# Performance work log

Measured on AMD Instinct MI355X. Metric: run time of the kernel, lower is better.

Reference implementation:

```python
import jax, jax.numpy as jnp
import numpy as np

HIDDEN = 2048
INTER = 7168
N_EXPERTS = 8
BATCH, SEQ, TOP_K = 1, 2048, 2


def setup_inputs() -> dict:
    key = jax.random.key(0)
    ks = jax.random.split(key, 6)
    x = jax.random.normal(ks[0], (BATCH, SEQ, HIDDEN), dtype=jnp.float32)
    expert_indices = jax.random.randint(ks[1], (BATCH, SEQ, TOP_K), 0, N_EXPERTS, dtype=jnp.int64)
    expert_weights = jax.random.uniform(ks[2], (BATCH, SEQ, TOP_K), dtype=jnp.float32)
    gate_proj = jax.random.normal(ks[3], (N_EXPERTS, INTER, HIDDEN), dtype=jnp.float32) * 0.02
    up_proj = jax.random.normal(ks[4], (N_EXPERTS, INTER, HIDDEN), dtype=jnp.float32) * 0.02
    down_proj = jax.random.normal(ks[5], (N_EXPERTS, HIDDEN, INTER), dtype=jnp.float32) * 0.02
    return {"x": x, "expert_indices": expert_indices, "expert_weights": expert_weights,
            "gate_proj": gate_proj, "up_proj": up_proj, "down_proj": down_proj}


def reference(x, expert_indices, expert_weights, gate_proj, up_proj, down_proj):
    B, S, H = x.shape
    E = gate_proj.shape[0]
    T = B * S
    xf = x.reshape(T, H)
    # Per-token combine weight for each expert: sum router weights over the
    # top-k slots that picked that expert.  comb: [T, E]
    onehot = jax.nn.one_hot(expert_indices.reshape(T, -1), E, dtype=x.dtype)  # [T, K, E]
    comb = jnp.einsum('tke,tk->te', onehot, expert_weights.reshape(T, -1))
    out = jnp.zeros((T, H), dtype=x.dtype)
    for e in range(E):  # small fixed loop over experts (structurally distinct weights)
        g = xf @ gate_proj[e].T            # [T, I]
        u = xf @ up_proj[e].T              # [T, I]
        h = g * jax.nn.sigmoid(g) * u      # SwiGLU (silu(gate) * up)
        out = out + (h @ down_proj[e].T) * comb[:, e:e + 1]
    return out.reshape(B, S, H)
```

## Files before the change

### kernel.cpp

```cpp
#include <hip/hip_runtime.h>
#include <hip/hip_bf16.h>
#include <math.h>

#define HDIM 2048
#define IDIM 7168
#define NEXP 8
#define TTOK 2048
#define TOPK 2
#define NASSIGN (TTOK * TOPK)
#define ROWCAP 5120

#define BK 32
#define LDK 40

typedef float  f32x4 __attribute__((ext_vector_type(4)));
typedef int    i32x4 __attribute__((ext_vector_type(4)));
typedef unsigned short u16;
typedef u16    u16x8 __attribute__((ext_vector_type(8)));

__device__ __forceinline__ u16 f2bf(float f) {
    return __builtin_bit_cast(u16, (__bf16)f);
}

__device__ __forceinline__ f32x4 mfma16(i32x4 a, i32x4 b, f32x4 c) {
    asm("v_mfma_f32_16x16x32_bf16 %0, %1, %2, %0" : "+v"(c) : "v"(a), "v"(b));
    return c;
}

__device__ __forceinline__ void cvt_store8(u16* dst, f32x4 a, f32x4 b) {
    u16x8 p;
    p[0]=f2bf(a[0]); p[1]=f2bf(a[1]); p[2]=f2bf(a[2]); p[3]=f2bf(a[3]);
    p[4]=f2bf(b[0]); p[5]=f2bf(b[1]); p[6]=f2bf(b[2]); p[7]=f2bf(b[3]);
    *(u16x8*)dst = p;
}

__device__ __forceinline__ void stage16(u16* dst, const float* src) {
    const f32x4* s = (const f32x4*)src;
    f32x4 v0 = s[0], v1 = s[1];
    cvt_store8(dst, v0, v1);
    f32x4 v2 = s[2], v3 = s[3];
    cvt_store8(dst + 8, v2, v3);
}

__global__ void route_kernel(const int* __restrict__ idx,
                             const float* __restrict__ w,
                             int* __restrict__ cnt, int* __restrict__ poff,
                             int* __restrict__ tok, float* __restrict__ wgt) {
    __shared__ int s_cnt[NEXP];
    __shared__ int s_off[NEXP + 1];
    __shared__ int s_cur[NEXP];
    int tid = threadIdx.x;
    if (tid < NEXP) { s_cnt[tid] = 0; s_cur[tid] = 0; }
    __syncthreads();
    for (int a = tid; a < NASSIGN; a += blockDim.x)
        atomicAdd(&s_cnt[idx[a]], 1);
    for (int i = tid; i < ROWCAP; i += blockDim.x) { tok[i] = 0; wgt[i] = 0.0f; }
    __syncthreads();
    if (tid == 0) {
        int o = 0;
        for (int e = 0; e < NEXP; ++e) { s_off[e] = o; o += (s_cnt[e] + 127) & ~127; }
        s_off[NEXP] = o;
    }
    __syncthreads();
    for (int a = tid; a < NASSIGN; a += blockDim.x) {
        int e = idx[a];
        int slot = atomicAdd(&s_cur[e], 1);
        int p = s_off[e] + slot;
        tok[p] = a >> 1;
        wgt[p] = w[a];
    }
    if (tid < NEXP) cnt[tid] = s_cnt[tid];
    if (tid <= NEXP) poff[tid] = s_off[tid];
}

__global__ __launch_bounds__(256) void
moe_gateup_kernel(const float* __restrict__ x,
                  const float* __restrict__ gate,
                  const float* __restrict__ up,
                  const int* __restrict__ poff,
                  const int* __restrict__ tok,
                  u16* __restrict__ hbuf) {
    int e    = blockIdx.z;
    int base = poff[e];
    int pc   = poff[e + 1] - base;
    int m0   = blockIdx.y * 128;
    if (m0 >= pc) return;
    int n0 = blockIdx.x * 128;

    __shared__ __align__(16) u16 As[128][LDK];
    __shared__ __align__(16) u16 Bg[128][LDK];
    __shared__ __align__(16) u16 Bu[128][LDK];

    int tid  = threadIdx.x;
    int srow = tid >> 1;
    int scol = (tid & 1) * 16;

    int t = tok[base + m0 + srow];
    const float* pa = x    + (size_t)t * HDIM + scol;
    const float* pg = gate + ((size_t)e * IDIM + (n0 + srow)) * (size_t)HDIM + scol;
    const float* pu = up   + ((size_t)e * IDIM + (n0 + srow)) * (size_t)HDIM + scol;

    int lane = tid & 63;
    int wv   = tid >> 6;
    int wr   = (wv >> 1) * 64;
    int wc   = (wv & 1) * 64;
    int fr   = lane & 15;
    int fk   = (lane >> 4) * 8;

    f32x4 accg[4][4], accu[4][4];
#pragma unroll
    for (int i = 0; i < 4; ++i)
#pragma unroll
        for (int j = 0; j < 4; ++j) { accg[i][j] = (f32x4)0.0f; accu[i][j] = (f32x4)0.0f; }

    for (int k0 = 0; k0 < HDIM; k0 += BK) {
        __syncthreads();
        stage16(&As[srow][scol], pa + k0);
        stage16(&Bg[srow][scol], pg + k0);
        stage16(&Bu[srow][scol], pu + k0);
        __syncthreads();

        i32x4 af[4], bg[4], bu[4];
#pragma unroll
        for (int mf = 0; mf < 4; ++mf) af[mf] = *(const i32x4*)&As[wr + mf * 16 + fr][fk];
#pragma unroll
        for (int nf = 0; nf < 4; ++nf) {
            bg[nf] = *(const i32x4*)&Bg[wc + nf * 16 + fr][fk];
            bu[nf] = *(const i32x4*)&Bu[wc + nf * 16 + fr][fk];
        }
#pragma unroll
        for (int mf = 0; mf < 4; ++mf)
#pragma unroll
            for (int nf = 0; nf < 4; ++nf) {
                accg[mf][nf] = mfma16(af[mf], bg[nf], accg[mf][nf]);
                accu[mf][nf] = mfma16(af[mf], bu[nf], accu[mf][nf]);
            }
    }

#pragma unroll
    for (int mf = 0; mf < 4; ++mf) {
#pragma unroll
        for (int j = 0; j < 4; ++j) {
            int row = wr + mf * 16 + (lane >> 4) * 4 + j;
            size_t hrow = (size_t)(base + m0 + row);
#pragma unroll
            for (int nf = 0; nf < 4; ++nf) {
                float g = accg[mf][nf][j];
                float u = accu[mf][nf][j];
                float sg = 1.0f / (1.0f + __expf(-g));
                float hv = g * sg * u;
                int col = n0 + wc + nf * 16 + fr;
                hbuf[hrow * IDIM + col] = f2bf(hv);
            }
        }
    }
}

__global__ __launch_bounds__(256) void
moe_down_kernel(const u16* __restrict__ hbuf,
                const float* __restrict__ down,
                const int* __restrict__ poff,
                const int* __restrict__ tok,
                const float* __restrict__ wgt,
                float* __restrict__ out) {
    int e    = blockIdx.z;
    int base = poff[e];
    int pc   = poff[e + 1] - base;
    int m0   = blockIdx.y * 128;
    if (m0 >= pc) return;
    int n0 = blockIdx.x * 128;

    __shared__ __align__(16) u16 Ah[128][LDK];
    __shared__ __align__(16) u16 Bd[128][LDK];

    int tid  = threadIdx.x;
    int srow = tid >> 1;
    int scol = (tid & 1) * 16;

    const u16*   ph = hbuf + (size_t)(base + m0 + srow) * IDIM + scol;
    const float* pd = down + ((size_t)e * HDIM + (n0 + srow)) * (size_t)IDIM + scol;

    int lane = tid & 63;
    int wv   = tid >> 6;
    int wr   = (wv >> 1) * 64;
    int wc   = (wv & 1) * 64;
    int fr   = lane & 15;
    int fk   = (lane >> 4) * 8;

    f32x4 acc[4][4];
#pragma unroll
    for (int i = 0; i < 4; ++i)
#pragma unroll
        for (int j = 0; j < 4; ++j) acc[i][j] = (f32x4)0.0f;

    for (int k0 = 0; k0 < IDIM; k0 += BK) {
        __syncthreads();
        *(u16x8*)&Ah[srow][scol]     = *(const u16x8*)(ph + k0);
        *(u16x8*)&Ah[srow][scol + 8] = *(const u16x8*)(ph + k0 + 8);
        stage16(&Bd[srow][scol], pd + k0);
        __syncthreads();

        i32x4 af[4], bf[4];
#pragma unroll
        for (int mf = 0; mf < 4; ++mf) af[mf] = *(const i32x4*)&Ah[wr + mf * 16 + fr][fk];
#pragma unroll
        for (int nf = 0; nf < 4; ++nf) bf[nf] = *(const i32x4*)&Bd[wc + nf * 16 + fr][fk];
#pragma unroll
        for (int mf = 0; mf < 4; ++mf)
#pragma unroll
            for (int nf = 0; nf < 4; ++nf)
                acc[mf][nf] = mfma16(af[mf], bf[nf], acc[mf][nf]);
    }

#pragma unroll
    for (int mf = 0; mf < 4; ++mf) {
#pragma unroll
        for (int j = 0; j < 4; ++j) {
            int row = wr + mf * 16 + (lane >> 4) * 4 + j;
            int hr  = base + m0 + row;
            int t   = tok[hr];
            float w = wgt[hr];
            if (w != 0.0f) {
#pragma unroll
                for (int nf = 0; nf < 4; ++nf) {
                    int col = n0 + wc + nf * 16 + fr;
                    atomicAdd(&out[(size_t)t * HDIM + col], acc[mf][nf][j] * w);
                }
            }
        }
    }
}

extern "C" void kernel_launch(void* const* d_in, const int* in_sizes, int n_in,
                              void* d_out, int out_size, void* d_ws, size_t ws_size,
                              hipStream_t stream) {
    const float* x    = (const float*)d_in[0];
    const int*   eidx = (const int*)d_in[1];
    const float* ew   = (const float*)d_in[2];
    const float* gate = (const float*)d_in[3];
    const float* up   = (const float*)d_in[4];
    const float* down = (const float*)d_in[5];
    float* out = (float*)d_out;

    char* ws   = (char*)d_ws;
    int*  cnt  = (int*)ws;
    int*  poff = (int*)(ws + 64);
    int*  tok  = (int*)(ws + 1024);
    float* wgt = (float*)(ws + 1024 + ROWCAP * 4);
    u16*  hbuf = (u16*)(ws + 65536);

    route_kernel<<<1, 256, 0, stream>>>(eidx, ew, cnt, poff, tok, wgt);
    hipMemsetAsync(d_out, 0, (size_t)TTOK * HDIM * sizeof(float), stream);

    dim3 gA(IDIM / 128, 32, NEXP);
    moe_gateup_kernel<<<gA, 256, 0, stream>>>(x, gate, up, poff, tok, hbuf);

    dim3 gB(HDIM / 128, 32, NEXP);
    moe_down_kernel<<<gB, 256, 0, stream>>>(hbuf, down, poff, tok, wgt, out);
}
```

Before: 1.263 ms.

## Pre-convert inputs and weights to bf16 and stage tiles with direct global-to-LDS loads

Adds a conversion kernel that turns x and the gate, up and down weights into bf16 copies in the workspace on every call. The GEMM kernels then stage tiles with global_load_lds into an XOR-swizzled, unpadded LDS layout instead of loading fp32 and converting in registers. The aim is to cut redundant fp32 weight reads and the per-tile conversion ALU work inside the GEMM loops. In exchange every call pays extra full passes over the weights, about 1.4 GB of fp32 reads plus bf16 writes, and it needs a large workspace; the old fp32 kernels remain as a fallback when the workspace is too small.

```diff
diff --git a/kernel.cpp b/kernel.cpp
--- a/kernel.cpp
+++ b/kernel.cpp
@@ -9,7 +9,6 @@
 #define TOPK 2
 #define NASSIGN (TTOK * TOPK)
 #define ROWCAP 5120
-
 #define BK 32
 #define LDK 40
 
@@ -26,6 +25,10 @@
     asm("v_mfma_f32_16x16x32_bf16 %0, %1, %2, %0" : "+v"(c) : "v"(a), "v"(b));
     return c;
 }
+
+#define GLD(gsrc, ldst) __builtin_amdgcn_global_load_lds( \
+    (const __attribute__((address_space(1))) void*)(gsrc), \
+    (__attribute__((address_space(3))) void*)(ldst), 16, 0, 0)
 
 __device__ __forceinline__ void cvt_store8(u16* dst, f32x4 a, f32x4 b) {
     u16x8 p;
@@ -73,13 +76,29 @@
     if (tid <= NEXP) poff[tid] = s_off[tid];
 }
 
+__global__ __launch_bounds__(256) void cvt_bf16_kernel(const float* __restrict__ src,
+                                                       u16* __restrict__ dst,
+                                                       long long n8) {
+    long long i = (long long)blockIdx.x * blockDim.x + threadIdx.x;
+    long long stride = (long long)gridDim.x * blockDim.x;
+    for (; i < n8; i += stride) {
+        const f32x4* s = (const f32x4*)(src + i * 8);
+        f32x4 a = s[0], b = s[1];
+        u16x8 p;
+        p[0]=f2bf(a[0]); p[1]=f2bf(a[1]); p[2]=f2bf(a[2]); p[3]=f2bf(a[3]);
+        p[4]=f2bf(b[0]); p[5]=f2bf(b[1]); p[6]=f2bf(b[2]); p[7]=f2bf(b[3]);
+        *(u16x8*)(dst + i * 8) = p;
+    }
+}
+
+
 __global__ __launch_bounds__(256) void
-moe_gateup_kernel(const float* __restrict__ x,
-                  const float* __restrict__ gate,
-                  const float* __restrict__ up,
-                  const int* __restrict__ poff,
-                  const int* __restrict__ tok,
-                  u16* __restrict__ hbuf) {
+moe_gateup_bf16(const u16* __restrict__ xbf,
+                const u16* __restrict__ gbf,
+                const u16* __restrict__ ubf,
+                const int* __restrict__ poff,
+                const int* __restrict__ tok,
+                u16* __restrict__ hbuf) {
     int e    = blockIdx.z;
     int base = poff[e];
     int pc   = poff[e + 1] - base;
@@ -87,25 +106,44 @@
     if (m0 >= pc) return;
     int n0 = blockIdx.x * 128;
 
-    __shared__ __align__(16) u16 As[128][LDK];
-    __shared__ __align__(16) u16 Bg[128][LDK];
-    __shared__ __align__(16) u16 Bu[128][LDK];
-
-    int tid  = threadIdx.x;
-    int srow = tid >> 1;
-    int scol = (tid & 1) * 16;
-
-    int t = tok[base + m0 + srow];
-    const float* pa = x    + (size_t)t * HDIM + scol;
-    const float* pg = gate + ((size_t)e * IDIM + (n0 + srow)) * (size_t)HDIM + scol;
-    const float* pu = up   + ((size_t)e * IDIM + (n0 + srow)) * (size_t)HDIM + scol;
+    __shared__ __align__(16) u16 As[128 * 32];
+    __shared__ __align__(16) u16 Bg[128 * 32];
+    __shared__ __align__(16) u16 Bu[128 * 32];
+
+    int tid = threadIdx.x;
+    int r0 = tid >> 2, s0 = tid & 3;
+    int r1 = r0 + 64;
+    int c0 = s0 ^ ((r0 >> 1) & 3);
+    int c1 = s0 ^ ((r1 >> 1) & 3);
+
+    const u16* pa0 = xbf + (size_t)tok[base + m0 + r0] * HDIM + c0 * 8;
+    const u16* pa1 = xbf + (size_t)tok[base + m0 + r1] * HDIM + c1 * 8;
+    const u16* pg0 = gbf + ((size_t)e * IDIM + n0 + r0) * HDIM + c0 * 8;
+    const u16* pg1 = gbf + ((size_t)e * IDIM + n0 + r1) * HDIM + c1 * 8;
+    const u16* pu0 = ubf + ((size_t)e * IDIM + n0 + r0) * HDIM + c0 * 8;
+    const u16* pu1 = ubf + ((size_t)e * IDIM + n0 + r1) * HDIM + c1 * 8;
+    u16* lA0 = &As[tid * 8]; u16* lA1 = &As[(tid + 256) * 8];
+    u16* lG0 = &Bg[tid * 8]; u16* lG1 = &Bg[(tid + 256) * 8];
+    u16* lU0 = &Bu[tid * 8]; u16* lU1 = &Bu[(tid + 256) * 8];
 
     int lane = tid & 63;
     int wv   = tid >> 6;
     int wr   = (wv >> 1) * 64;
     int wc   = (wv & 1) * 64;
     int fr   = lane & 15;
-    int fk   = (lane >> 4) * 8;
+    int cc   = lane >> 4;
+
+    int offA[4], offB[4];
+#pragma unroll
+    for (int mf = 0; mf < 4; ++mf) {
+        int R = wr + mf * 16 + fr;
+        offA[mf] = R * 32 + (cc ^ ((R >> 1) & 3)) * 8;
+    }
+#pragma unroll
+    for (int nf = 0; nf < 4; ++nf) {
+        int R = wc + nf * 16 + fr;
+        offB[nf] = R * 32 + (cc ^ ((R >> 1) & 3)) * 8;
+    }
 
     f32x4 accg[4][4], accu[4][4];
 #pragma unroll
@@ -115,18 +153,19 @@
 
     for (int k0 = 0; k0 < HDIM; k0 += BK) {
         __syncthreads();
-        stage16(&As[srow][scol], pa + k0);
-        stage16(&Bg[srow][scol], pg + k0);
-        stage16(&Bu[srow][scol], pu + k0);
+        GLD(pa0, lA0); GLD(pa1, lA1);
+        GLD(pg0, lG0); GLD(pg1, lG1);
+        GLD(pu0, lU0); GLD(pu1, lU1);
+        pa0 += BK; pa1 += BK; pg0 += BK; pg1 += BK; pu0 += BK; pu1 += BK;
         __syncthreads();
 
         i32x4 af[4], bg[4], bu[4];
 #pragma unroll
-        for (int mf = 0; mf < 4; ++mf) af[mf] = *(const i32x4*)&As[wr + mf * 16 + fr][fk];
+        for (int mf = 0; mf < 4; ++mf) af[mf] = *(const i32x4*)&As[offA[mf]];
 #pragma unroll
         for (int nf = 0; nf < 4; ++nf) {
-            bg[nf] = *(const i32x4*)&Bg[wc + nf * 16 + fr][fk];
-            bu[nf] = *(const i32x4*)&Bu[wc + nf * 16 + fr][fk];
+            bg[nf] = *(const i32x4*)&Bg[offB[nf]];
+            bu[nf] = *(const i32x4*)&Bu[offB[nf]];
         }
 #pragma unroll
         for (int mf = 0; mf < 4; ++mf)
@@ -148,21 +187,19 @@
                 float g = accg[mf][nf][j];
                 float u = accu[mf][nf][j];
                 float sg = 1.0f / (1.0f + __expf(-g));
-                float hv = g * sg * u;
-                int col = n0 + wc + nf * 16 + fr;
-                hbuf[hrow * IDIM + col] = f2bf(hv);
+                hbuf[hrow * IDIM + n0 + wc + nf * 16 + fr] = f2bf(g * sg * u);
             }
         }
     }
 }
 
 __global__ __launch_bounds__(256) void
-moe_down_kernel(const u16* __restrict__ hbuf,
-                const float* __restrict__ down,
-                const int* __restrict__ poff,
-                const int* __restrict__ tok,
-                const float* __restrict__ wgt,
-                float* __restrict__ out) {
+moe_down_bf16(const u16* __restrict__ hbuf,
+              const u16* __restrict__ dbf,
+              const int* __restrict__ poff,
+              const int* __restrict__ tok,
+              const float* __restrict__ wgt,
+              float* __restrict__ out) {
     int e    = blockIdx.z;
     int base = poff[e];
     int pc   = poff[e + 1] - base;
@@ -170,22 +207,40 @@
     if (m0 >= pc) return;
     int n0 = blockIdx.x * 128;
 
-    __shared__ __align__(16) u16 Ah[128][LDK];
-    __shared__ __align__(16) u16 Bd[128][LDK];
-
-    int tid  = threadIdx.x;
-    int srow = tid >> 1;
-    int scol = (tid & 1) * 16;
-
-    const u16*   ph = hbuf + (size_t)(base + m0 + srow) * IDIM + scol;
-    const float* pd = down + ((size_t)e * HDIM + (n0 + srow)) * (size_t)IDIM + scol;
+    __shared__ __align__(16) u16 Ah[128 * 32];
+    __shared__ __align__(16) u16 Bd[128 * 32];
+
+    int tid = threadIdx.x;
+    int r0 = tid >> 2, s0 = tid & 3;
+    int r1 = r0 + 64;
+    int c0 = s0 ^ ((r0 >> 1) & 3);
+    int c1 = s0 ^ ((r1 >> 1) & 3);
+
+    const u16* ph0 = hbuf + (size_t)(base + m0 + r0) * IDIM + c0 * 8;
+    const u16* ph1 = hbuf + (size_t)(base + m0 + r1) * IDIM + c1 * 8;
+    const u16* pd0 = dbf + ((size_t)e * HDIM + n0 + r0) * IDIM + c0 * 8;
+    const u16* pd1 = dbf + ((size_t)e * HDIM + n0 + r1) * IDIM + c1 * 8;
+    u16* lA0 = &Ah[tid * 8]; u16* lA1 = &Ah[(tid + 256) * 8];
+    u16* lB0 = &Bd[tid * 8]; u16* lB1 = &Bd[(tid + 256) * 8];
 
     int lane = tid & 63;
     int wv   = tid >> 6;
     int wr   = (wv >> 1) * 64;
     int wc   = (wv & 1) * 64;
     int fr   = lane & 15;
-    int fk   = (lane >> 4) * 8;
+    int cc   = lane >> 4;
+
+    int offA[4], offB[4];
+#pragma unroll
+    for (int mf = 0; mf < 4; ++mf) {
+        int R = wr + mf * 16 + fr;
+        offA[mf] = R * 32 + (cc ^ ((R >> 1) & 3)) * 8;
+    }
+#pragma unroll
+    for (int nf = 0; nf < 4; ++nf) {
+        int R = wc + nf * 16 + fr;
+        offB[nf] = R * 32 + (cc ^ ((R >> 1) & 3)) * 8;
+    }
 
     f32x4 acc[4][4];
 #pragma unroll
@@ -195,21 +250,21 @@
 
     for (int k0 = 0; k0 < IDIM; k0 += BK) {
         __syncthreads();
-        *(u16x8*)&Ah[srow][scol]     = *(const u16x8*)(ph + k0);
-        *(u16x8*)&Ah[srow][scol + 8] = *(const u16x8*)(ph + k0 + 8);
-        stage16(&Bd[srow][scol], pd + k0);
-        __syncthreads();
-
-        i32x4 af[4], bf[4];
-#pragma unroll
-        for (int mf = 0; mf < 4; ++mf) af[mf] = *(const i32x4*)&Ah[wr + mf * 16 + fr][fk];
-#pragma unroll
-        for (int nf = 0; nf < 4; ++nf) bf[nf] = *(const i32x4*)&Bd[wc + nf * 16 + fr][fk];
+        GLD(ph0, lA0); GLD(ph1, lA1);
+        GLD(pd0, lB0); GLD(pd1, lB1);
+        ph0 += BK; ph1 += BK; pd0 += BK; pd1 += BK;
+        __syncthreads();
+
+        i32x4 af[4], bf_[4];
+#pragma unroll
+        for (int mf = 0; mf < 4; ++mf) af[mf] = *(const i32x4*)&Ah[offA[mf]];
+#pragma unroll
+        for (int nf = 0; nf < 4; ++nf) bf_[nf] = *(const i32x4*)&Bd[offB[nf]];
 #pragma unroll
         for (int mf = 0; mf < 4; ++mf)
 #pragma unroll
             for (int nf = 0; nf < 4; ++nf)
-                acc[mf][nf] = mfma16(af[mf], bf[nf], acc[mf][nf]);
+                acc[mf][nf] = mfma16(af[mf], bf_[nf], acc[mf][nf]);
     }
 
 #pragma unroll
@@ -219,6 +274,140 @@
             int row = wr + mf * 16 + (lane >> 4) * 4 + j;
             int hr  = base + m0 + row;
             int t   = tok[hr];
+            float w = wgt[hr];
+            if (w != 0.0f) {
+#pragma unroll
+                for (int nf = 0; nf < 4; ++nf) {
+                    int col = n0 + wc + nf * 16 + fr;
+                    atomicAdd(&out[(size_t)t * HDIM + col], acc[mf][nf][j] * w);
+                }
+            }
+        }
+    }
+}
+
+__global__ __launch_bounds__(256) void
+moe_gateup_f32(const float* __restrict__ x, const float* __restrict__ gate,
+               const float* __restrict__ up, const int* __restrict__ poff,
+               const int* __restrict__ tok, u16* __restrict__ hbuf) {
+    int e = blockIdx.z;
+    int base = poff[e];
+    int pc = poff[e + 1] - base;
+    int m0 = blockIdx.y * 128;
+    if (m0 >= pc) return;
+    int n0 = blockIdx.x * 128;
+    __shared__ __align__(16) u16 As[128][LDK];
+    __shared__ __align__(16) u16 Bg[128][LDK];
+    __shared__ __align__(16) u16 Bu[128][LDK];
+    int tid = threadIdx.x;
+    int srow = tid >> 1;
+    int scol = (tid & 1) * 16;
+    int t = tok[base + m0 + srow];
+    const float* pa = x + (size_t)t * HDIM + scol;
+    const float* pg = gate + ((size_t)e * IDIM + (n0 + srow)) * (size_t)HDIM + scol;
+    const float* pu = up + ((size_t)e * IDIM + (n0 + srow)) * (size_t)HDIM + scol;
+    int lane = tid & 63;
+    int wv = tid >> 6;
+    int wr = (wv >> 1) * 64;
+    int wc = (wv & 1) * 64;
+    int fr = lane & 15;
+    int fk = (lane >> 4) * 8;
+    f32x4 accg[4][4], accu[4][4];
+#pragma unroll
+    for (int i = 0; i < 4; ++i)
+#pragma unroll
+        for (int j = 0; j < 4; ++j) { accg[i][j] = (f32x4)0.0f; accu[i][j] = (f32x4)0.0f; }
+    for (int k0 = 0; k0 < HDIM; k0 += BK) {
+        __syncthreads();
+        stage16(&As[srow][scol], pa + k0);
+        stage16(&Bg[srow][scol], pg + k0);
+        stage16(&Bu[srow][scol], pu + k0);
+        __syncthreads();
+        i32x4 af[4], bg[4], bu[4];
+#pragma unroll
+        for (int mf = 0; mf < 4; ++mf) af[mf] = *(const i32x4*)&As[wr + mf * 16 + fr][fk];
+#pragma unroll
+        for (int nf = 0; nf < 4; ++nf) {
+            bg[nf] = *(const i32x4*)&Bg[wc + nf * 16 + fr][fk];
+            bu[nf] = *(const i32x4*)&Bu[wc + nf * 16 + fr][fk];
+        }
+#pragma unroll
+        for (int mf = 0; mf < 4; ++mf)
+#pragma unroll
+            for (int nf = 0; nf < 4; ++nf) {
+                accg[mf][nf] = mfma16(af[mf], bg[nf], accg[mf][nf]);
+                accu[mf][nf] = mfma16(af[mf], bu[nf], accu[mf][nf]);
+            }
+    }
+#pragma unroll
+    for (int mf = 0; mf < 4; ++mf) {
+#pragma unroll
+        for (int j = 0; j < 4; ++j) {
+            int row = wr + mf * 16 + (lane >> 4) * 4 + j;
+            size_t hrow = (size_t)(base + m0 + row);
+#pragma unroll
+            for (int nf = 0; nf < 4; ++nf) {
+                float g = accg[mf][nf][j];
+                float u = accu[mf][nf][j];
+                float sg = 1.0f / (1.0f + __expf(-g));
+                hbuf[hrow * IDIM + n0 + wc + nf * 16 + fr] = f2bf(g * sg * u);
+            }
+        }
+    }
+}
+
+__global__ __launch_bounds__(256) void
+moe_down_f32(const u16* __restrict__ hbuf, const float* __restrict__ down,
+             const int* __restrict__ poff, const int* __restrict__ tok,
+             const float* __restrict__ wgt, float* __restrict__ out) {
+    int e = blockIdx.z;
+    int base = poff[e];
+    int pc = poff[e + 1] - base;
+    int m0 = blockIdx.y * 128;
+    if (m0 >= pc) return;
+    int n0 = blockIdx.x * 128;
+    __shared__ __align__(16) u16 Ah[128][LDK];
+    __shared__ __align__(16) u16 Bd[128][LDK];
+    int tid = threadIdx.x;
+    int srow = tid >> 1;
+    int scol = (tid & 1) * 16;
+    const u16* ph = hbuf + (size_t)(base + m0 + srow) * IDIM + scol;
+    const float* pd = down + ((size_t)e * HDIM + (n0 + srow)) * (size_t)IDIM + scol;
+    int lane = tid & 63;
+    int wv = tid >> 6;
+    int wr = (wv >> 1) * 64;
+    int wc = (wv & 1) * 64;
+    int fr = lane & 15;
+    int fk = (lane >> 4) * 8;
+    f32x4 acc[4][4];
+#pragma unroll
+    for (int i = 0; i < 4; ++i)
+#pragma unroll
+        for (int j = 0; j < 4; ++j) acc[i][j] = (f32x4)0.0f;
+    for (int k0 = 0; k0 < IDIM; k0 += BK) {
+        __syncthreads();
+        *(u16x8*)&Ah[srow][scol] = *(const u16x8*)(ph + k0);
+        *(u16x8*)&Ah[srow][scol + 8] = *(const u16x8*)(ph + k0 + 8);
+        stage16(&Bd[srow][scol], pd + k0);
+        __syncthreads();
+        i32x4 af[4], bf_[4];
+#pragma unroll
+        for (int mf = 0; mf < 4; ++mf) af[mf] = *(const i32x4*)&Ah[wr + mf * 16 + fr][fk];
+#pragma unroll
+        for (int nf = 0; nf < 4; ++nf) bf_[nf] = *(const i32x4*)&Bd[wc + nf * 16 + fr][fk];
+#pragma unroll
+        for (int mf = 0; mf < 4; ++mf)
+#pragma unroll
+            for (int nf = 0; nf < 4; ++nf)
+                acc[mf][nf] = mfma16(af[mf], bf_[nf], acc[mf][nf]);
+    }
+#pragma unroll
+    for (int mf = 0; mf < 4; ++mf) {
+#pragma unroll
+        for (int j = 0; j < 4; ++j) {
+            int row = wr + mf * 16 + (lane >> 4) * 4 + j;
+            int hr = base + m0 + row;
+            int t = tok[hr];
             float w = wgt[hr];
             if (w != 0.0f) {
 #pragma unroll
@@ -247,14 +436,43 @@
     int*  poff = (int*)(ws + 64);
     int*  tok  = (int*)(ws + 1024);
     float* wgt = (float*)(ws + 1024 + ROWCAP * 4);
-    u16*  hbuf = (u16*)(ws + 65536);
+
+    const size_t xbf_sz = (size_t)TTOK * HDIM * 2;
+    const size_t w_sz   = (size_t)NEXP * IDIM * HDIM * 2;
+    const size_t h_sz   = (size_t)ROWCAP * IDIM * 2;
+    const size_t xbf_off = 65536;
+    const size_t g_off   = xbf_off + xbf_sz;
+    const size_t u_off   = g_off + w_sz;
+    const size_t h_off   = u_off + w_sz;
+    const size_t need    = h_off + h_sz;
 
     route_kernel<<<1, 256, 0, stream>>>(eidx, ew, cnt, poff, tok, wgt);
     hipMemsetAsync(d_out, 0, (size_t)TTOK * HDIM * sizeof(float), stream);
 
-    dim3 gA(IDIM / 128, 32, NEXP);
-    moe_gateup_kernel<<<gA, 256, 0, stream>>>(x, gate, up, poff, tok, hbuf);
-
-    dim3 gB(HDIM / 128, 32, NEXP);
-    moe_down_kernel<<<gB, 256, 0, stream>>>(hbuf, down, poff, tok, wgt, out);
-}
+    if (ws_size >= need) {
+        u16* xbf = (u16*)(ws + xbf_off);
+        u16* gbf = (u16*)(ws + g_off);
+        u16* ubf = (u16*)(ws + u_off);
+        u16* hb  = (u16*)(ws + h_off);
+        u16* dbf = gbf;
+
+        long long nw8 = (long long)NEXP * IDIM * HDIM / 8;
+        cvt_bf16_kernel<<<1024, 256, 0, stream>>>(x, xbf, (long long)TTOK * HDIM / 8);
+        cvt_bf16_kernel<<<2048, 256, 0, stream>>>(gate, gbf, nw8);
+        cvt_bf16_kernel<<<2048, 256, 0, stream>>>(up, ubf, nw8);
+
+        dim3 gA(IDIM / 128, 32, NEXP);
+        moe_gateup_bf16<<<gA, 256, 0, stream>>>(xbf, gbf, ubf, poff, tok, hb);
+
+        cvt_bf16_kernel<<<2048, 256, 0, stream>>>(down, dbf, nw8);
+
+        dim3 gB(HDIM / 128, 32, NEXP);
+        moe_down_bf16<<<gB, 256, 0, stream>>>(hb, dbf, poff, tok, wgt, out);
+    } else {
+        u16* hb = (u16*)(ws + 65536);
+        dim3 gA(IDIM / 128, 32, NEXP);
+        moe_gateup_f32<<<gA, 256, 0, stream>>>(x, gate, up, poff, tok, hb);
+        dim3 gB(HDIM / 128, 32, NEXP);
+        moe_down_f32<<<gB, 256, 0, stream>>>(hb, down, poff, tok, wgt, out);
+    }
+}
```

Result: faster. 1.069 ms (-15.3%).
